# Performance work log

Measured on AMD Instinct MI355X. Metric: run time of the kernel, lower is better.

The kernel has to match this reference:

```python
import jax, jax.numpy as jnp
import numpy as np

N = 8192        # n_nodes
F = 256         # n_features
RES_H = 512     # n_res_hidden
REP_H = 256     # n_rep_hidden
EMB = 128       # embed_dim
E = 262144      # n_edges
GAMMA = 0.1


def setup_inputs() -> dict:
    key = jax.random.key(0)
    ks = jax.random.split(key, 20)
    w = lambda k, shape, s=0.05: (jax.random.normal(k, shape, jnp.float32) * s)
    return {
        "x": jax.random.normal(ks[0], (N, F), jnp.float32),
        "edge_index": jax.random.randint(ks[1], (2, E), 0, N),
        # res_model: Linear(N,RES_H)+ReLU, Linear(RES_H,F)+ReLU
        "res_W1": w(ks[2], (N, RES_H)), "res_b1": jnp.zeros((RES_H,), jnp.float32),
        "res_W2": w(ks[3], (RES_H, F)), "res_b2": jnp.zeros((F,), jnp.float32),
        "fc_W1": w(ks[4], (F, REP_H)), "fc_b1": jnp.zeros((REP_H,), jnp.float32),
        "fc_W2": w(ks[5], (REP_H, REP_H)), "fc_b2": jnp.zeros((REP_H,), jnp.float32),
        # rep_gcn: GCNConv(F,REP_H,norm=False), GCNConv(REP_H,REP_H), GCNConv(REP_H,EMB)
        "g_W0": w(ks[6], (F, REP_H)), "g_b0": jnp.zeros((REP_H,), jnp.float32),
        "g_W1": w(ks[7], (REP_H, REP_H)), "g_b1": jnp.zeros((REP_H,), jnp.float32),
        "g_W2": w(ks[8], (REP_H, EMB)), "g_b2": jnp.zeros((EMB,), jnp.float32),
        # dec_fc: Linear(EMB,REP_H)+ReLU, Linear(REP_H,F)+ReLU
        "dec_W1": w(ks[9], (EMB, REP_H)), "dec_b1": jnp.zeros((REP_H,), jnp.float32),
        "dec_W2": w(ks[10], (REP_H, F)), "dec_b2": jnp.zeros((F,), jnp.float32),
    }


def _gcn(h, src, dst, W, b, normalize):
    """PyG GCNConv: transform then aggregate src->dst; sym-norm with self loops if normalize."""
    h = h @ W
    if normalize:
        ones = jnp.ones(src.shape[0], h.dtype)
        deg = jax.ops.segment_sum(ones, dst, num_segments=N) + 1.0  # +1 self loop
        dinv = jax.lax.rsqrt(deg)
        coef = dinv[src] * dinv[dst]
        agg = jax.ops.segment_sum(h[src] * coef[:, None], dst, num_segments=N)
        agg = agg + h * (dinv * dinv)[:, None]  # self-loop message
    else:
        agg = jax.ops.segment_sum(h[src], dst, num_segments=N)
    return agg + b


def _fwd(x, edge_index, res_W1, res_b1, res_W2, res_b2, fc_W1, fc_b1, fc_W2, fc_b2,
         g_W0, g_b0, g_W1, g_b1, g_W2, g_b2, dec_W1, dec_b1, dec_W2, dec_b2):
    relu = jax.nn.relu
    src, dst = edge_index[0], edge_index[1]
    # dense adjacency (to_dense_adj accumulates edge weights = 1)
    A = jnp.zeros((N, N), x.dtype).at[src, dst].add(1.0)
    # residual model over adjacency rows
    R = relu(relu(A @ res_W1 + res_b1) @ res_W2 + res_b2)  # [N, F]
    # GCN layer 0 (normalize=False)
    H = relu(_gcn(x, src, dst, g_W0, g_b0, False))
    # layer 1
    R_l = relu(R @ fc_W1 + fc_b1)
    H = relu(_gcn(H * jnp.exp(-GAMMA * R_l), src, dst, g_W1, g_b1, True))
    # layer 2
    R_l = relu(R_l @ fc_W2 + fc_b2)
    H = relu(_gcn(H * jnp.exp(-GAMMA * R_l), src, dst, g_W2, g_b2, True))  # [N, EMB]
    X_hat = relu(relu(H @ dec_W1 + dec_b1) @ dec_W2 + dec_b2)  # [N, F]
    A_hat = H @ H.T  # [N, N]
    return X_hat, A_hat, R


def reference(x, edge_index, res_W1, res_b1, res_W2, res_b2, fc_W1, fc_b1, fc_W2, fc_b2,
              g_W0, g_b0, g_W1, g_b1, g_W2, g_b2, dec_W1, dec_b1, dec_W2, dec_b2):
    return _fwd(x, edge_index, res_W1, res_b1, res_W2, res_b2, fc_W1, fc_b1, fc_W2, fc_b2,
                g_W0, g_b0, g_W1, g_b1, g_W2, g_b2, dec_W1, dec_b1, dec_W2, dec_b2)
```

## Files before the change

### kernel.cpp

```cpp
#include <hip/hip_runtime.h>
#include <cstddef>
#include <cstdint>

#define NN   8192
#define FF   256
#define RESH 512
#define REPH 256
#define EMBD 128
#define EE   262144
#define GAMMA_ 0.1f


__global__ void count_kernel(const int* __restrict__ ei, int* __restrict__ cnt_src,
                             int* __restrict__ cnt_dst) {
  int e = blockIdx.x * blockDim.x + threadIdx.x;
  if (e < EE) {
    atomicAdd(&cnt_src[ei[e]], 1);
    atomicAdd(&cnt_dst[ei[EE + e]], 1);
  }
}

__global__ void scan_kernel(const int* __restrict__ cnt_src, const int* __restrict__ cnt_dst,
                            int* __restrict__ off_src, int* __restrict__ off_dst) {
  const int* cnt = blockIdx.x ? cnt_dst : cnt_src;
  int* off = blockIdx.x ? off_dst : off_src;
  __shared__ int sm[1024];
  int carry = 0;
  for (int ch = 0; ch < NN / 1024; ++ch) {
    int idx = ch * 1024 + threadIdx.x;
    int v = cnt[idx];
    int x = v;
    sm[threadIdx.x] = x;
    __syncthreads();
    for (int ofs = 1; ofs < 1024; ofs <<= 1) {
      int y = (threadIdx.x >= ofs) ? sm[threadIdx.x - ofs] : 0;
      __syncthreads();
      x += y;
      sm[threadIdx.x] = x;
      __syncthreads();
    }
    off[idx] = x - v + carry;
    carry += sm[1023];
    __syncthreads();
  }
  if (threadIdx.x == 0) off[NN] = carry;
}

__global__ void fill_kernel(const int* __restrict__ ei, const int* __restrict__ off_src,
                            const int* __restrict__ off_dst, int* __restrict__ cur_src,
                            int* __restrict__ cur_dst, int* __restrict__ adj_src,
                            int* __restrict__ adj_dst) {
  int e = blockIdx.x * blockDim.x + threadIdx.x;
  if (e < EE) {
    int s = ei[e], d = ei[EE + e];
    int ps = atomicAdd(&cur_src[s], 1);
    adj_src[off_src[s] + ps] = d;
    int pd = atomicAdd(&cur_dst[d], 1);
    adj_dst[off_dst[d] + pd] = s;
  }
}

__global__ void dinv_kernel(const int* __restrict__ cnt_dst, float* __restrict__ dinv) {
  int n = blockIdx.x * blockDim.x + threadIdx.x;
  if (n < NN) dinv[n] = rsqrtf((float)cnt_dst[n] + 1.0f);
}

__global__ __launch_bounds__(256) void s1_kernel(const float* __restrict__ W1,
    const float* __restrict__ b1, const int* __restrict__ off_src,
    const int* __restrict__ adj_src, float* __restrict__ S1) {
  int i = blockIdx.x, t = threadIdx.x;
  int beg = off_src[i], end = off_src[i + 1];
  float a0 = 0.f, a1 = 0.f;
  for (int k = beg; k < end; ++k) {
    int d = adj_src[k];
    const float* row = W1 + (size_t)d * RESH;
    a0 += row[t];
    a1 += row[t + 256];
  }
  S1[(size_t)i * RESH + t]       = fmaxf(a0 + b1[t], 0.f);
  S1[(size_t)i * RESH + t + 256] = fmaxf(a1 + b1[t + 256], 0.f);
}

__global__ __launch_bounds__(256) void agg0_kernel(const float* __restrict__ h,
    const float* __restrict__ b, const int* __restrict__ off_dst,
    const int* __restrict__ adj_dst, float* __restrict__ out) {
  int d = blockIdx.x, t = threadIdx.x;
  int beg = off_dst[d], end = off_dst[d + 1];
  float acc = 0.f;
  for (int k = beg; k < end; ++k) {
    int s = adj_dst[k];
    acc += h[(size_t)s * REPH + t];
  }
  out[(size_t)d * REPH + t] = fmaxf(acc + b[t], 0.f);
}

__global__ void aggn_kernel(const float* __restrict__ h, const float* __restrict__ b,
    const float* __restrict__ dinv, const int* __restrict__ off_dst,
    const int* __restrict__ adj_dst, float* __restrict__ out, int C) {
  int d = blockIdx.x, t = threadIdx.x;
  int beg = off_dst[d], end = off_dst[d + 1];
  float acc = 0.f;
  for (int k = beg; k < end; ++k) {
    int s = adj_dst[k];
    acc += h[(size_t)s * C + t] * dinv[s];
  }
  float dd = dinv[d];
  float v = acc * dd + h[(size_t)d * C + t] * dd * dd + b[t];
  out[(size_t)d * C + t] = fmaxf(v, 0.f);
}

__global__ void mod_kernel(const float* __restrict__ h, const float* __restrict__ r,
                           float* __restrict__ out, int n) {
  int i = blockIdx.x * blockDim.x + threadIdx.x;
  if (i < n) out[i] = h[i] * expf(-GAMMA_ * r[i]);
}

__global__ __launch_bounds__(256) void gemm64(const float* __restrict__ A,
    const float* __restrict__ B, const float* __restrict__ bias, float* __restrict__ C,
    int M, int K, int Nc, int doRelu) {
  __shared__ float As[16][68];
  __shared__ float Bs[16][68];
  int t = threadIdx.x;
  int tx = t & 15, ty = t >> 4;
  int bm = blockIdx.y * 64, bn = blockIdx.x * 64;
  float acc[4][4] = {};
  for (int k0 = 0; k0 < K; k0 += 16) {
#pragma unroll
    for (int i = 0; i < 4; ++i) {
      int lin = t + i * 256;
      int r = lin >> 4, c = lin & 15;
      As[c][r] = A[(size_t)(bm + r) * K + k0 + c];
    }
#pragma unroll
    for (int i = 0; i < 4; ++i) {
      int lin = t + i * 256;
      int r = lin >> 6, c = lin & 63;
      Bs[r][c] = B[(size_t)(k0 + r) * Nc + bn + c];
    }
    __syncthreads();
#pragma unroll
    for (int k = 0; k < 16; ++k) {
      float a[4], b[4];
#pragma unroll
      for (int i = 0; i < 4; ++i) a[i] = As[k][ty * 4 + i];
#pragma unroll
      for (int j = 0; j < 4; ++j) b[j] = Bs[k][tx * 4 + j];
#pragma unroll
      for (int i = 0; i < 4; ++i)
#pragma unroll
        for (int j = 0; j < 4; ++j) acc[i][j] += a[i] * b[j];
    }
    __syncthreads();
  }
#pragma unroll
  for (int i = 0; i < 4; ++i) {
    size_t r = (size_t)(bm + ty * 4 + i);
    int c0 = bn + tx * 4;
    float4 v;
    v.x = acc[i][0]; v.y = acc[i][1]; v.z = acc[i][2]; v.w = acc[i][3];
    if (bias) {
      v.x += bias[c0 + 0]; v.y += bias[c0 + 1]; v.z += bias[c0 + 2]; v.w += bias[c0 + 3];
    }
    if (doRelu) {
      v.x = fmaxf(v.x, 0.f); v.y = fmaxf(v.y, 0.f); v.z = fmaxf(v.z, 0.f); v.w = fmaxf(v.w, 0.f);
    }
    *(float4*)(&C[r * Nc + c0]) = v;
  }
}

__global__ __launch_bounds__(256) void ahat64(const float* __restrict__ H,
                                              float* __restrict__ C) {
  __shared__ float As[16][68];
  __shared__ float Bs[16][68];
  int t = threadIdx.x;
  int tx = t & 15, ty = t >> 4;
  int bi = blockIdx.y * 64, bj = blockIdx.x * 64;
  float acc[4][4] = {};
  for (int k0 = 0; k0 < EMBD; k0 += 16) {
#pragma unroll
    for (int i = 0; i < 4; ++i) {
      int lin = t + i * 256;
      int r = lin >> 4, c = lin & 15;
      As[c][r] = H[(size_t)(bi + r) * EMBD + k0 + c];
      Bs[c][r] = H[(size_t)(bj + r) * EMBD + k0 + c];
    }
    __syncthreads();
#pragma unroll
    for (int k = 0; k < 16; ++k) {
      float a[4], b[4];
#pragma unroll
      for (int i = 0; i < 4; ++i) a[i] = As[k][ty * 4 + i];
#pragma unroll
      for (int j = 0; j < 4; ++j) b[j] = Bs[k][tx * 4 + j];
#pragma unroll
      for (int i = 0; i < 4; ++i)
#pragma unroll
        for (int j = 0; j < 4; ++j) acc[i][j] += a[i] * b[j];
    }
    __syncthreads();
  }
#pragma unroll
  for (int i = 0; i < 4; ++i) {
    size_t r = (size_t)(bi + ty * 4 + i);
    float4 v;
    v.x = acc[i][0]; v.y = acc[i][1]; v.z = acc[i][2]; v.w = acc[i][3];
    *(float4*)(&C[r * NN + bj + tx * 4]) = v;
  }
}


extern "C" void kernel_launch(void* const* d_in, const int* in_sizes, int n_in,
                              void* d_out, int out_size, void* d_ws, size_t ws_size,
                              hipStream_t stream) {
  const float* x      = (const float*)d_in[0];
  const int*   ei     = (const int*)d_in[1];
  const float* res_W1 = (const float*)d_in[2];
  const float* res_b1 = (const float*)d_in[3];
  const float* res_W2 = (const float*)d_in[4];
  const float* res_b2 = (const float*)d_in[5];
  const float* fc_W1  = (const float*)d_in[6];
  const float* fc_b1  = (const float*)d_in[7];
  const float* fc_W2  = (const float*)d_in[8];
  const float* fc_b2  = (const float*)d_in[9];
  const float* g_W0   = (const float*)d_in[10];
  const float* g_b0   = (const float*)d_in[11];
  const float* g_W1   = (const float*)d_in[12];
  const float* g_b1   = (const float*)d_in[13];
  const float* g_W2   = (const float*)d_in[14];
  const float* g_b2   = (const float*)d_in[15];
  const float* dec_W1 = (const float*)d_in[16];
  const float* dec_b1 = (const float*)d_in[17];
  const float* dec_W2 = (const float*)d_in[18];
  const float* dec_b2 = (const float*)d_in[19];

  float* out   = (float*)d_out;
  float* X_hat = out;
  float* A_hat = out + (size_t)NN * FF;
  float* R     = A_hat + (size_t)NN * NN;

  char* ws = (char*)d_ws;
  size_t o = 0;
  auto alloc = [&](size_t bytes) -> void* {
    void* p = ws + o;
    o += (bytes + 1023) & ~(size_t)1023;
    return p;
  };
  int* cnt_src = (int*)alloc(NN * 4);
  int* cnt_dst = (int*)alloc(NN * 4);
  int* cur_src = (int*)alloc(NN * 4);
  int* cur_dst = (int*)alloc(NN * 4);
  int* off_src = (int*)alloc((NN + 1) * 4);
  int* off_dst = (int*)alloc((NN + 1) * 4);
  int* adj_src = (int*)alloc((size_t)EE * 4);
  int* adj_dst = (int*)alloc((size_t)EE * 4);
  float* dinv  = (float*)alloc(NN * 4);
  float* S1    = (float*)alloc((size_t)NN * RESH * 4);
  float* B1    = (float*)alloc((size_t)NN * REPH * 4);
  float* B2    = (float*)alloc((size_t)NN * REPH * 4);
  float* B3    = (float*)alloc((size_t)NN * REPH * 4);
  float* B4    = (float*)alloc((size_t)NN * REPH * 4);

  hipMemsetAsync(cnt_src, 0, (size_t)NN * 4 * 4, stream);

  count_kernel<<<EE / 256, 256, 0, stream>>>(ei, cnt_src, cnt_dst);
  scan_kernel<<<2, 1024, 0, stream>>>(cnt_src, cnt_dst, off_src, off_dst);
  fill_kernel<<<EE / 256, 256, 0, stream>>>(ei, off_src, off_dst, cur_src, cur_dst,
                                            adj_src, adj_dst);
  dinv_kernel<<<NN / 256, 256, 0, stream>>>(cnt_dst, dinv);

  s1_kernel<<<NN, 256, 0, stream>>>(res_W1, res_b1, off_src, adj_src, S1);
  gemm64<<<dim3(FF / 64, NN / 64), 256, 0, stream>>>(S1, res_W2, res_b2, R, NN, RESH, FF, 1);
  gemm64<<<dim3(REPH / 64, NN / 64), 256, 0, stream>>>(x, g_W0, nullptr, B1, NN, FF, REPH, 0);
  agg0_kernel<<<NN, REPH, 0, stream>>>(B1, g_b0, off_dst, adj_dst, B2);
  gemm64<<<dim3(REPH / 64, NN / 64), 256, 0, stream>>>(R, fc_W1, fc_b1, B3, NN, FF, REPH, 1);
  mod_kernel<<<(NN * REPH) / 256, 256, 0, stream>>>(B2, B3, B1, NN * REPH);
  gemm64<<<dim3(REPH / 64, NN / 64), 256, 0, stream>>>(B1, g_W1, nullptr, B2, NN, REPH, REPH, 0);
  aggn_kernel<<<NN, REPH, 0, stream>>>(B2, g_b1, dinv, off_dst, adj_dst, B1, REPH);
  gemm64<<<dim3(REPH / 64, NN / 64), 256, 0, stream>>>(B3, fc_W2, fc_b2, B4, NN, REPH, REPH, 1);
  mod_kernel<<<(NN * REPH) / 256, 256, 0, stream>>>(B1, B4, B2, NN * REPH);
  gemm64<<<dim3(EMBD / 64, NN / 64), 256, 0, stream>>>(B2, g_W2, nullptr, B3, NN, REPH, EMBD, 0);
  aggn_kernel<<<NN, EMBD, 0, stream>>>(B3, g_b2, dinv, off_dst, adj_dst, B4, EMBD);
  gemm64<<<dim3(REPH / 64, NN / 64), 256, 0, stream>>>(B4, dec_W1, dec_b1, B1, NN, EMBD, REPH, 1);
  gemm64<<<dim3(FF / 64, NN / 64), 256, 0, stream>>>(B1, dec_W2, dec_b2, X_hat, NN, REPH, FF, 1);
  ahat64<<<dim3(NN / 64, NN / 64), 256, 0, stream>>>(B4, A_hat);
}
```

Measured before the change: 941.7 us.

## Use split-bf16 MFMA GEMMs with fused exp modulation and MFMA A_hat

Replaces the FP32 SIMT tiled GEMMs with MFMA bf16 kernels that split each fp32 operand into high and low bf16 parts and accumulate three products, keeping close to fp32 accuracy. Weights are pre-transposed and split once per call, and H is split before the A_hat product. The exp(-gamma*R) modulation is fused into the GEMM A-operand load, removing the separate mod kernels. Gather loops get unroll pragmas. The GEMMs read operands directly from global memory without LDS staging, which may limit reuse, and the A_hat output is written as scalar stores that may coalesce poorly.

```diff
diff --git a/kernel.cpp b/kernel.cpp
--- a/kernel.cpp
+++ b/kernel.cpp
@@ -9,6 +9,20 @@
 #define EMBD 128
 #define EE   262144
 #define GAMMA_ 0.1f
+
+typedef __attribute__((ext_vector_type(8))) short bf16x8;
+typedef __attribute__((ext_vector_type(4))) float f32x4;
+
+__device__ inline void f2hilo(float x, short& h, short& l) {
+  unsigned u = __float_as_uint(x);
+  unsigned r = u + 0x7FFFu + ((u >> 16) & 1u);
+  h = (short)(r >> 16);
+  float hf = __uint_as_float(r & 0xFFFF0000u);
+  float lf = x - hf;
+  unsigned u2 = __float_as_uint(lf);
+  unsigned r2 = u2 + 0x7FFFu + ((u2 >> 16) & 1u);
+  l = (short)(r2 >> 16);
+}
 
 
 __global__ void count_kernel(const int* __restrict__ ei, int* __restrict__ cnt_src,
@@ -71,6 +85,7 @@
   int i = blockIdx.x, t = threadIdx.x;
   int beg = off_src[i], end = off_src[i + 1];
   float a0 = 0.f, a1 = 0.f;
+#pragma unroll 4
   for (int k = beg; k < end; ++k) {
     int d = adj_src[k];
     const float* row = W1 + (size_t)d * RESH;
@@ -87,6 +102,7 @@
   int d = blockIdx.x, t = threadIdx.x;
   int beg = off_dst[d], end = off_dst[d + 1];
   float acc = 0.f;
+#pragma unroll 4
   for (int k = beg; k < end; ++k) {
     int s = adj_dst[k];
     acc += h[(size_t)s * REPH + t];
@@ -100,6 +116,7 @@
   int d = blockIdx.x, t = threadIdx.x;
   int beg = off_dst[d], end = off_dst[d + 1];
   float acc = 0.f;
+#pragma unroll 4
   for (int k = beg; k < end; ++k) {
     int s = adj_dst[k];
     acc += h[(size_t)s * C + t] * dinv[s];
@@ -109,103 +126,128 @@
   out[(size_t)d * C + t] = fmaxf(v, 0.f);
 }
 
-__global__ void mod_kernel(const float* __restrict__ h, const float* __restrict__ r,
-                           float* __restrict__ out, int n) {
-  int i = blockIdx.x * blockDim.x + threadIdx.x;
-  if (i < n) out[i] = h[i] * expf(-GAMMA_ * r[i]);
-}
-
-__global__ __launch_bounds__(256) void gemm64(const float* __restrict__ A,
-    const float* __restrict__ B, const float* __restrict__ bias, float* __restrict__ C,
-    int M, int K, int Nc, int doRelu) {
-  __shared__ float As[16][68];
-  __shared__ float Bs[16][68];
-  int t = threadIdx.x;
-  int tx = t & 15, ty = t >> 4;
-  int bm = blockIdx.y * 64, bn = blockIdx.x * 64;
-  float acc[4][4] = {};
-  for (int k0 = 0; k0 < K; k0 += 16) {
-#pragma unroll
-    for (int i = 0; i < 4; ++i) {
-      int lin = t + i * 256;
-      int r = lin >> 4, c = lin & 15;
-      As[c][r] = A[(size_t)(bm + r) * K + k0 + c];
-    }
-#pragma unroll
-    for (int i = 0; i < 4; ++i) {
-      int lin = t + i * 256;
-      int r = lin >> 6, c = lin & 63;
-      Bs[r][c] = B[(size_t)(k0 + r) * Nc + bn + c];
-    }
-    __syncthreads();
-#pragma unroll
-    for (int k = 0; k < 16; ++k) {
-      float a[4], b[4];
-#pragma unroll
-      for (int i = 0; i < 4; ++i) a[i] = As[k][ty * 4 + i];
-#pragma unroll
-      for (int j = 0; j < 4; ++j) b[j] = Bs[k][tx * 4 + j];
-#pragma unroll
-      for (int i = 0; i < 4; ++i)
-#pragma unroll
-        for (int j = 0; j < 4; ++j) acc[i][j] += a[i] * b[j];
-    }
-    __syncthreads();
-  }
-#pragma unroll
-  for (int i = 0; i < 4; ++i) {
-    size_t r = (size_t)(bm + ty * 4 + i);
-    int c0 = bn + tx * 4;
-    float4 v;
-    v.x = acc[i][0]; v.y = acc[i][1]; v.z = acc[i][2]; v.w = acc[i][3];
-    if (bias) {
-      v.x += bias[c0 + 0]; v.y += bias[c0 + 1]; v.z += bias[c0 + 2]; v.w += bias[c0 + 3];
-    }
-    if (doRelu) {
-      v.x = fmaxf(v.x, 0.f); v.y = fmaxf(v.y, 0.f); v.z = fmaxf(v.z, 0.f); v.w = fmaxf(v.w, 0.f);
-    }
-    *(float4*)(&C[r * Nc + c0]) = v;
-  }
-}
-
-__global__ __launch_bounds__(256) void ahat64(const float* __restrict__ H,
-                                              float* __restrict__ C) {
-  __shared__ float As[16][68];
-  __shared__ float Bs[16][68];
-  int t = threadIdx.x;
-  int tx = t & 15, ty = t >> 4;
-  int bi = blockIdx.y * 64, bj = blockIdx.x * 64;
-  float acc[4][4] = {};
-  for (int k0 = 0; k0 < EMBD; k0 += 16) {
-#pragma unroll
-    for (int i = 0; i < 4; ++i) {
-      int lin = t + i * 256;
-      int r = lin >> 4, c = lin & 15;
-      As[c][r] = H[(size_t)(bi + r) * EMBD + k0 + c];
-      Bs[c][r] = H[(size_t)(bj + r) * EMBD + k0 + c];
-    }
-    __syncthreads();
-#pragma unroll
-    for (int k = 0; k < 16; ++k) {
-      float a[4], b[4];
-#pragma unroll
-      for (int i = 0; i < 4; ++i) a[i] = As[k][ty * 4 + i];
-#pragma unroll
-      for (int j = 0; j < 4; ++j) b[j] = Bs[k][tx * 4 + j];
-#pragma unroll
-      for (int i = 0; i < 4; ++i)
-#pragma unroll
-        for (int j = 0; j < 4; ++j) acc[i][j] += a[i] * b[j];
-    }
-    __syncthreads();
-  }
-#pragma unroll
-  for (int i = 0; i < 4; ++i) {
-    size_t r = (size_t)(bi + ty * 4 + i);
-    float4 v;
-    v.x = acc[i][0]; v.y = acc[i][1]; v.z = acc[i][2]; v.w = acc[i][3];
-    *(float4*)(&C[r * NN + bj + tx * 4]) = v;
-  }
+struct WDesc { const float* src; short* h; short* l; int K; int N; };
+struct WTab { WDesc d[8]; };
+
+__global__ void prep_w(WTab tab) {
+  WDesc d = tab.d[blockIdx.y];
+  int total = d.K * d.N;
+  for (int i = blockIdx.x * 256 + threadIdx.x; i < total; i += 128 * 256) {
+    int n = i / d.K, k = i - n * d.K;
+    float x = d.src[(size_t)k * d.N + n];
+    short hh, ll;
+    f2hilo(x, hh, ll);
+    d.h[i] = hh;
+    d.l[i] = ll;
+  }
+}
+
+__global__ void conv_h(const float* __restrict__ Hf, short* __restrict__ Hh,
+                       short* __restrict__ Hl) {
+  int i = blockIdx.x * 256 + threadIdx.x;
+  float x = Hf[i];
+  short hh, ll;
+  f2hilo(x, hh, ll);
+  Hh[i] = hh;
+  Hl[i] = ll;
+}
+
+__global__ __launch_bounds__(256) void gemmW(const float* __restrict__ A,
+    const float* __restrict__ Rm, const short* __restrict__ Wh,
+    const short* __restrict__ Wl, const float* __restrict__ bias,
+    float* __restrict__ C, int K, int Nc, int doRelu) {
+  const int w = threadIdx.x >> 6, l = threadIdx.x & 63;
+  const int lr = l & 15, lk = l >> 4;
+  const int m0 = blockIdx.y * 64 + w * 16;
+  const int n0 = blockIdx.x * 128;
+  f32x4 acc[8] = {};
+  const int nks = K >> 5;
+  for (int ks = 0; ks < nks; ++ks) {
+    const int k0 = (ks << 5) + (lk << 3);
+    const float* ap = A + (size_t)(m0 + lr) * K + k0;
+    float av[8];
+    *(f32x4*)(av + 0) = *(const f32x4*)(ap + 0);
+    *(f32x4*)(av + 4) = *(const f32x4*)(ap + 4);
+    if (Rm) {
+      const float* rp = Rm + (size_t)(m0 + lr) * K + k0;
+      float rv[8];
+      *(f32x4*)(rv + 0) = *(const f32x4*)(rp + 0);
+      *(f32x4*)(rv + 4) = *(const f32x4*)(rp + 4);
+#pragma unroll
+      for (int j = 0; j < 8; ++j) av[j] *= expf(-GAMMA_ * rv[j]);
+    }
+    bf16x8 ah, al;
+#pragma unroll
+    for (int j = 0; j < 8; ++j) {
+      short hh, ll;
+      f2hilo(av[j], hh, ll);
+      ah[j] = hh;
+      al[j] = ll;
+    }
+#pragma unroll
+    for (int cb = 0; cb < 8; ++cb) {
+      size_t boff = (size_t)(n0 + (cb << 4) + lr) * K + k0;
+      bf16x8 bh = *(const bf16x8*)(Wh + boff);
+      bf16x8 bl = *(const bf16x8*)(Wl + boff);
+      acc[cb] = __builtin_amdgcn_mfma_f32_16x16x32_bf16(ah, bh, acc[cb], 0, 0, 0);
+      acc[cb] = __builtin_amdgcn_mfma_f32_16x16x32_bf16(al, bh, acc[cb], 0, 0, 0);
+      acc[cb] = __builtin_amdgcn_mfma_f32_16x16x32_bf16(ah, bl, acc[cb], 0, 0, 0);
+    }
+  }
+#pragma unroll
+  for (int cb = 0; cb < 8; ++cb) {
+    int col = n0 + (cb << 4) + lr;
+    float bv = bias ? bias[col] : 0.f;
+#pragma unroll
+    for (int r = 0; r < 4; ++r) {
+      int row = m0 + (lk << 2) + r;
+      float v = acc[cb][r] + bv;
+      if (doRelu) v = fmaxf(v, 0.f);
+      C[(size_t)row * Nc + col] = v;
+    }
+  }
+}
+
+__global__ __launch_bounds__(256) void ahat_mfma(const short* __restrict__ Hh,
+    const short* __restrict__ Hl, float* __restrict__ C) {
+  const int w = threadIdx.x >> 6, l = threadIdx.x & 63;
+  const int lr = l & 15, lk = l >> 4;
+  const int bi = blockIdx.y * 128 + w * 32;
+  const int bj = blockIdx.x * 128;
+  f32x4 acc[2][8] = {};
+#pragma unroll
+  for (int ks = 0; ks < 4; ++ks) {
+    const int k0 = (ks << 5) + (lk << 3);
+    bf16x8 ah[2], al[2];
+#pragma unroll
+    for (int rb = 0; rb < 2; ++rb) {
+      size_t off = (size_t)(bi + (rb << 4) + lr) * EMBD + k0;
+      ah[rb] = *(const bf16x8*)(Hh + off);
+      al[rb] = *(const bf16x8*)(Hl + off);
+    }
+#pragma unroll
+    for (int cb = 0; cb < 8; ++cb) {
+      size_t off = (size_t)(bj + (cb << 4) + lr) * EMBD + k0;
+      bf16x8 bh = *(const bf16x8*)(Hh + off);
+      bf16x8 bl = *(const bf16x8*)(Hl + off);
+#pragma unroll
+      for (int rb = 0; rb < 2; ++rb) {
+        acc[rb][cb] = __builtin_amdgcn_mfma_f32_16x16x32_bf16(ah[rb], bh, acc[rb][cb], 0, 0, 0);
+        acc[rb][cb] = __builtin_amdgcn_mfma_f32_16x16x32_bf16(al[rb], bh, acc[rb][cb], 0, 0, 0);
+        acc[rb][cb] = __builtin_amdgcn_mfma_f32_16x16x32_bf16(ah[rb], bl, acc[rb][cb], 0, 0, 0);
+      }
+    }
+  }
+#pragma unroll
+  for (int rb = 0; rb < 2; ++rb)
+#pragma unroll
+    for (int cb = 0; cb < 8; ++cb) {
+      int row = bi + (rb << 4) + (lk << 2);
+      int col = bj + (cb << 4) + lr;
+#pragma unroll
+      for (int r = 0; r < 4; ++r)
+        C[(size_t)(row + r) * NN + col] = acc[rb][cb][r];
+    }
 }
 
 
@@ -259,6 +301,19 @@
   float* B2    = (float*)alloc((size_t)NN * REPH * 4);
   float* B3    = (float*)alloc((size_t)NN * REPH * 4);
   float* B4    = (float*)alloc((size_t)NN * REPH * 4);
+  short* Wt_h  = (short*)alloc(524288 * 2);
+  short* Wt_l  = (short*)alloc(524288 * 2);
+  short* Hh    = (short*)alloc((size_t)NN * EMBD * 2);
+  short* Hl    = (short*)alloc((size_t)NN * EMBD * 2);
+
+  const int o_resW2 = 0;
+  const int o_fcW1  = 131072;
+  const int o_fcW2  = 196608;
+  const int o_gW0   = 262144;
+  const int o_gW1   = 327680;
+  const int o_gW2   = 393216;
+  const int o_decW1 = 425984;
+  const int o_decW2 = 458752;
 
   hipMemsetAsync(cnt_src, 0, (size_t)NN * 4 * 4, stream);
 
@@ -268,19 +323,37 @@
                                             adj_src, adj_dst);
   dinv_kernel<<<NN / 256, 256, 0, stream>>>(cnt_dst, dinv);
 
+  WTab tab;
+  tab.d[0] = {res_W2, Wt_h + o_resW2, Wt_l + o_resW2, RESH, FF};
+  tab.d[1] = {fc_W1,  Wt_h + o_fcW1,  Wt_l + o_fcW1,  FF,   REPH};
+  tab.d[2] = {fc_W2,  Wt_h + o_fcW2,  Wt_l + o_fcW2,  REPH, REPH};
+  tab.d[3] = {g_W0,   Wt_h + o_gW0,   Wt_l + o_gW0,   FF,   REPH};
+  tab.d[4] = {g_W1,   Wt_h + o_gW1,   Wt_l + o_gW1,   REPH, REPH};
+  tab.d[5] = {g_W2,   Wt_h + o_gW2,   Wt_l + o_gW2,   REPH, EMBD};
+  tab.d[6] = {dec_W1, Wt_h + o_decW1, Wt_l + o_decW1, EMBD, REPH};
+  tab.d[7] = {dec_W2, Wt_h + o_decW2, Wt_l + o_decW2, REPH, FF};
+  prep_w<<<dim3(128, 8), 256, 0, stream>>>(tab);
+
   s1_kernel<<<NN, 256, 0, stream>>>(res_W1, res_b1, off_src, adj_src, S1);
-  gemm64<<<dim3(FF / 64, NN / 64), 256, 0, stream>>>(S1, res_W2, res_b2, R, NN, RESH, FF, 1);
-  gemm64<<<dim3(REPH / 64, NN / 64), 256, 0, stream>>>(x, g_W0, nullptr, B1, NN, FF, REPH, 0);
+  gemmW<<<dim3(FF / 128, NN / 64), 256, 0, stream>>>(S1, nullptr, Wt_h + o_resW2,
+      Wt_l + o_resW2, res_b2, R, RESH, FF, 1);
+  gemmW<<<dim3(REPH / 128, NN / 64), 256, 0, stream>>>(x, nullptr, Wt_h + o_gW0,
+      Wt_l + o_gW0, nullptr, B1, FF, REPH, 0);
   agg0_kernel<<<NN, REPH, 0, stream>>>(B1, g_b0, off_dst, adj_dst, B2);
-  gemm64<<<dim3(REPH / 64, NN / 64), 256, 0, stream>>>(R, fc_W1, fc_b1, B3, NN, FF, REPH, 1);
-  mod_kernel<<<(NN * REPH) / 256, 256, 0, stream>>>(B2, B3, B1, NN * REPH);
-  gemm64<<<dim3(REPH / 64, NN / 64), 256, 0, stream>>>(B1, g_W1, nullptr, B2, NN, REPH, REPH, 0);
-  aggn_kernel<<<NN, REPH, 0, stream>>>(B2, g_b1, dinv, off_dst, adj_dst, B1, REPH);
-  gemm64<<<dim3(REPH / 64, NN / 64), 256, 0, stream>>>(B3, fc_W2, fc_b2, B4, NN, REPH, REPH, 1);
-  mod_kernel<<<(NN * REPH) / 256, 256, 0, stream>>>(B1, B4, B2, NN * REPH);
-  gemm64<<<dim3(EMBD / 64, NN / 64), 256, 0, stream>>>(B2, g_W2, nullptr, B3, NN, REPH, EMBD, 0);
-  aggn_kernel<<<NN, EMBD, 0, stream>>>(B3, g_b2, dinv, off_dst, adj_dst, B4, EMBD);
-  gemm64<<<dim3(REPH / 64, NN / 64), 256, 0, stream>>>(B4, dec_W1, dec_b1, B1, NN, EMBD, REPH, 1);
-  gemm64<<<dim3(FF / 64, NN / 64), 256, 0, stream>>>(B1, dec_W2, dec_b2, X_hat, NN, REPH, FF, 1);
-  ahat64<<<dim3(NN / 64, NN / 64), 256, 0, stream>>>(B4, A_hat);
-}
+  gemmW<<<dim3(REPH / 128, NN / 64), 256, 0, stream>>>(R, nullptr, Wt_h + o_fcW1,
+      Wt_l + o_fcW1, fc_b1, B3, FF, REPH, 1);
+  gemmW<<<dim3(REPH / 128, NN / 64), 256, 0, stream>>>(B2, B3, Wt_h + o_gW1,
+      Wt_l + o_gW1, nullptr, B1, REPH, REPH, 0);
+  aggn_kernel<<<NN, REPH, 0, stream>>>(B1, g_b1, dinv, off_dst, adj_dst, B2, REPH);
+  gemmW<<<dim3(REPH / 128, NN / 64), 256, 0, stream>>>(B3, nullptr, Wt_h + o_fcW2,
+      Wt_l + o_fcW2, fc_b2, B4, REPH, REPH, 1);
+  gemmW<<<dim3(EMBD / 128, NN / 64), 256, 0, stream>>>(B2, B4, Wt_h + o_gW2,
+      Wt_l + o_gW2, nullptr, B3, REPH, EMBD, 0);
+  aggn_kernel<<<NN, EMBD, 0, stream>>>(B3, g_b2, dinv, off_dst, adj_dst, B1, EMBD);
+  conv_h<<<(NN * EMBD) / 256, 256, 0, stream>>>(B1, Hh, Hl);
+  gemmW<<<dim3(REPH / 128, NN / 64), 256, 0, stream>>>(B1, nullptr, Wt_h + o_decW1,
+      Wt_l + o_decW1, dec_b1, B2, EMBD, REPH, 1);
+  gemmW<<<dim3(FF / 128, NN / 64), 256, 0, stream>>>(B2, nullptr, Wt_h + o_decW2,
+      Wt_l + o_decW2, dec_b2, X_hat, REPH, FF, 1);
+  ahat_mfma<<<dim3(NN / 128, NN / 128), 256, 0, stream>>>(Hh, Hl, A_hat);
+}
```

Measured after the change: 881.3 us. 6.4% less time.
